# Kernel optimization log

Hardware: AMD Instinct MI355X
Metric: run time of the kernel (lower is better)

Reference implementation:

```python
import jax, jax.numpy as jnp
import numpy as np

NEG_SLOPE = 0.2  # PyG GATConv default negative_slope


def gat_layer(x, edge_index, W, att_src, att_dst, bias):
    """GATConv with self-loops, concat heads. x:[N,F_in], W:[F_in,H*C]."""
    N = x.shape[0]
    H, C = att_src.shape
    loop = jnp.arange(N, dtype=edge_index.dtype)
    src = jnp.concatenate([edge_index[0], loop])  # [E+N]
    dst = jnp.concatenate([edge_index[1], loop])
    h = (x @ W).reshape(N, H, C)                  # [N,H,C]
    a_src = jnp.einsum('nhc,hc->nh', h, att_src)  # [N,H]
    a_dst = jnp.einsum('nhc,hc->nh', h, att_dst)
    e = a_src[src] + a_dst[dst]                   # [E+N,H]
    e = jnp.where(e > 0, e, NEG_SLOPE * e)        # leaky_relu
    # numerically-stable segment softmax over incoming edges of each dst node
    m = jax.ops.segment_max(e, dst, num_segments=N)           # [N,H]
    ex = jnp.exp(e - m[dst])
    denom = jax.ops.segment_sum(ex, dst, num_segments=N)      # [N,H]
    alpha = ex / (denom[dst] + 1e-16)                          # [E+N,H]
    out = jax.ops.segment_sum(h[src] * alpha[:, :, None], dst, num_segments=N)
    return out.reshape(N, H * C) + bias


def setup_inputs() -> dict:
    key = jax.random.key(0)
    ks = jax.random.split(key, 16)
    N, E, F_IN, HID, H, NCLS = 50000, 800000, 128, 64, 4, 40
    HC = H * HID
    s = 0.1
    return {
        'x': jax.random.normal(ks[0], (N, F_IN), jnp.float32),
        'edge_index': jax.random.randint(ks[1], (2, E), 0, N, jnp.int32),
        'W1': jax.random.normal(ks[2], (F_IN, HC), jnp.float32) * s,
        'att_src1': jax.random.normal(ks[3], (H, HID), jnp.float32) * s,
        'att_dst1': jax.random.normal(ks[4], (H, HID), jnp.float32) * s,
        'b1': jnp.zeros((HC,), jnp.float32),
        'W2': jax.random.normal(ks[5], (HC, HC), jnp.float32) * s,
        'att_src2': jax.random.normal(ks[6], (H, HID), jnp.float32) * s,
        'att_dst2': jax.random.normal(ks[7], (H, HID), jnp.float32) * s,
        'b2': jnp.zeros((HC,), jnp.float32),
        'fcW1': jax.random.normal(ks[8], (HC, HID), jnp.float32) * s,
        'fcb1': jnp.zeros((HID,), jnp.float32),
        'fcW2': jax.random.normal(ks[9], (HID, NCLS), jnp.float32) * s,
        'fcb2': jnp.zeros((NCLS,), jnp.float32),
    }


def reference(x, edge_index, W1, att_src1, att_dst1, b1,
              W2, att_src2, att_dst2, b2, fcW1, fcb1, fcW2, fcb2):
    h = gat_layer(x, edge_index, W1, att_src1, att_dst1, b1)
    h = jax.nn.elu(h)
    h = gat_layer(h, edge_index, W2, att_src2, att_dst2, b2)
    h = jax.nn.elu(h)
    h = jnp.maximum(h @ fcW1 + fcb1, 0.0)  # ReLU; dropout is identity in eval
    return h @ fcW2 + fcb2                 # [N, num_classes]
```

## Files before the change

kernel.cpp:

```cpp
#include <hip/hip_runtime.h>

typedef __attribute__((ext_vector_type(8))) _Float16 fp16x8;
typedef __attribute__((ext_vector_type(4))) float f32x4;
typedef unsigned int u32;

__device__ __forceinline__ float lrelu(float x) { return x > 0.f ? x : 0.2f * x; }
__device__ __forceinline__ float elu(float x) { return x > 0.f ? x : __expf(x) - 1.f; }

__device__ __forceinline__ void gl2lds16(const void* g, void* l) {
    __builtin_amdgcn_global_load_lds((const __attribute__((address_space(1))) u32*)g,
                                     (__attribute__((address_space(3))) u32*)l, 16, 0, 0);
}

__device__ __forceinline__ void t16t_body(const float* __restrict__ W, _Float16* __restrict__ T,
                                          int N, int Nreal, int t) {
    int lane = t & 63, rem = t >> 6;
    int kk = rem & 1; rem >>= 1;
    int ncg = N / 16;
    int cg = rem % ncg, kc = rem / ncg;
    int k = kc * 64 + kk * 32 + (lane >> 4) * 8;
    int n = cg * 16 + (lane & 15);
    fp16x8 o;
#pragma unroll
    for (int j = 0; j < 8; ++j)
        o[j] = (n < Nreal) ? (_Float16)W[(size_t)(k + j) * Nreal + n] : (_Float16)0.f;
    *(fp16x8*)(T + (size_t)t * 8) = o;
}

__global__ __launch_bounds__(256) void k_prep(const float* __restrict__ W1, _Float16* __restrict__ W1T,
                                              const float* __restrict__ W2, _Float16* __restrict__ W2T,
                                              const float* __restrict__ fcW1, _Float16* __restrict__ fWT,
                                              const float* __restrict__ fcW2, _Float16* __restrict__ f2T,
                                              const int* __restrict__ dst, int* __restrict__ cnt) {
    int b = blockIdx.x, tid = threadIdx.x;
    if (b < 16)      t16t_body(W1, W1T, 256, 256, b * 256 + tid);
    else if (b < 48) t16t_body(W2, W2T, 256, 256, (b - 16) * 256 + tid);
    else if (b < 56) t16t_body(fcW1, fWT, 64, 64, (b - 48) * 256 + tid);
    else if (b < 58) t16t_body(fcW2, f2T, 64, 40, (b - 56) * 256 + tid);
    else             atomicAdd(&cnt[dst[(b - 58) * 256 + tid]], 1);
}

__global__ __launch_bounds__(256) void k_scan_a(const int* __restrict__ cnt, int* __restrict__ s,
                                                int* __restrict__ partial, int N) {
    __shared__ int sh[256];
    int t = threadIdx.x, gid = blockIdx.x * 256 + t;
    sh[t] = gid < N ? cnt[gid] : 0;
    __syncthreads();
    for (int off = 1; off < 256; off <<= 1) {
        int add = (t >= off) ? sh[t - off] : 0;
        __syncthreads();
        sh[t] += add;
        __syncthreads();
    }
    if (gid < N) s[gid] = sh[t];
    if (t == 255) partial[blockIdx.x] = sh[255];
}
__global__ __launch_bounds__(256) void k_scan_bc(const int* __restrict__ s, const int* __restrict__ partial,
                                                 const int* __restrict__ cnt, int* __restrict__ row_ptr,
                                                 int* __restrict__ cursor, int* __restrict__ bcur, int N) {
    __shared__ int red[256];
    int t = threadIdx.x, bid = blockIdx.x;
    int a = 0;
    for (int i = t; i < bid; i += 256) a += partial[i];
    red[t] = a;
    __syncthreads();
    for (int off = 128; off; off >>= 1) {
        if (t < off) red[t] += red[t + off];
        __syncthreads();
    }
    int base = red[0];
    int gid = bid * 256 + t;
    if (gid >= N) return;
    int val = s[gid] + base;
    row_ptr[gid + 1] = val;
    int excl = val - cnt[gid];
    cursor[gid] = excl;
    if ((gid & 511) == 0) bcur[gid >> 9] = excl;
    if (gid == 0) row_ptr[0] = 0;
}

__global__ __launch_bounds__(256) void k_bin(const int* __restrict__ src, const int* __restrict__ dst,
                                             int* __restrict__ bcur, int2* __restrict__ pairbuf, int E) {
    __shared__ int cnt[128], gbase[128], excl[128], cur2[128], sh[128];
    __shared__ int saddr[1024];
    __shared__ int2 spair[1024];
    const int tid = threadIdx.x;
    const int eb = blockIdx.x * 1024;
    if (tid < 128) { cnt[tid] = 0; cur2[tid] = 0; }
    __syncthreads();
    int s_[4], d_[4];
#pragma unroll
    for (int j = 0; j < 4; ++j) {
        int e = eb + j * 256 + tid;
        if (e < E) {
            s_[j] = src[e]; d_[j] = dst[e];
            atomicAdd(&cnt[d_[j] >> 9], 1);
        } else d_[j] = -1;
    }
    __syncthreads();
    if (tid < 128) sh[tid] = cnt[tid];
    __syncthreads();
    for (int off = 1; off < 128; off <<= 1) {
        int add = 0;
        if (tid < 128 && tid >= off) add = sh[tid - off];
        __syncthreads();
        if (tid < 128) sh[tid] += add;
        __syncthreads();
    }
    if (tid < 128) {
        excl[tid] = sh[tid] - cnt[tid];
        if (cnt[tid] > 0) gbase[tid] = atomicAdd(&bcur[tid], cnt[tid]);
    }
    __syncthreads();
#pragma unroll
    for (int j = 0; j < 4; ++j) {
        if (d_[j] >= 0) {
            int b = d_[j] >> 9;
            int r = atomicAdd(&cur2[b], 1);
            int slot = excl[b] + r;
            spair[slot] = make_int2(s_[j], d_[j]);
            saddr[slot] = gbase[b] + r;
        }
    }
    __syncthreads();
    int tot = min(1024, E - eb);
#pragma unroll
    for (int j = 0; j < 4; ++j) {
        int slot = j * 256 + tid;
        if (slot < tot) pairbuf[saddr[slot]] = spair[slot];
    }
}

template<int KV, int NW, int ATT, int AFP32>
__device__ __forceinline__ void gemm_body(int bid,
              const _Float16* __restrict__ Ah, const float* __restrict__ Af,
              const _Float16* __restrict__ BT, _Float16* __restrict__ Chi,
              const float* __restrict__ att_s, const float* __restrict__ att_d,
              float* __restrict__ a_src, float* __restrict__ a_dst,
              int M, int Nc) {
    constexpr int NCG = NW / 16;
    constexpr int CHUNK = NW * 64;
    constexpr int FPW = (CHUNK / 512) / 8;
    __shared__ _Float16 Bs[CHUNK];
    const int m0 = bid * 128;
    const int tid = threadIdx.x;
    const int lane = tid & 63, wv = tid >> 6;
    const int r16 = lane & 15, quad = lane >> 4;
    const int arow = min(m0 + wv * 16 + r16, M - 1);

    f32x4 acc[NCG];
#pragma unroll
    for (int cg = 0; cg < NCG; ++cg) acc[cg] = (f32x4){0, 0, 0, 0};

    constexpr int NCH = KV / 64;
#pragma unroll
    for (int kc = 0; kc < NCH; ++kc) {
        if (kc) __syncthreads();
#pragma unroll
        for (int f = 0; f < FPW; ++f) {
            int fr = wv * FPW + f;
            gl2lds16(BT + (size_t)kc * CHUNK + fr * 512 + lane * 8, &Bs[fr * 512]);
        }
        fp16x8 ar[2];
        if (AFP32) {
            const float* Ap = Af + (size_t)arow * KV + kc * 64 + quad * 8;
#pragma unroll
            for (int kk = 0; kk < 2; ++kk) {
                float4 u0 = *(const float4*)(Ap + kk * 32);
                float4 u1 = *(const float4*)(Ap + kk * 32 + 4);
                fp16x8 h8;
                h8[0] = (_Float16)u0.x; h8[1] = (_Float16)u0.y;
                h8[2] = (_Float16)u0.z; h8[3] = (_Float16)u0.w;
                h8[4] = (_Float16)u1.x; h8[5] = (_Float16)u1.y;
                h8[6] = (_Float16)u1.z; h8[7] = (_Float16)u1.w;
                ar[kk] = h8;
            }
        } else {
            const _Float16* Ahp = Ah + (size_t)arow * KV + kc * 64 + quad * 8;
#pragma unroll
            for (int kk = 0; kk < 2; ++kk) ar[kk] = *(const fp16x8*)(Ahp + kk * 32);
        }
        __syncthreads();
#pragma unroll
        for (int kk = 0; kk < 2; ++kk) {
#pragma unroll
            for (int cg = 0; cg < NCG; ++cg) {
                fp16x8 bh = *(const fp16x8*)(&Bs[(cg * 2 + kk) * 512 + lane * 8]);
                acc[cg] = __builtin_amdgcn_mfma_f32_16x16x32_f16(ar[kk], bh, acc[cg], 0, 0, 0);
            }
        }
    }

    const int rbase = m0 + wv * 16 + quad * 4;

    if (ATT) {
#pragma unroll
        for (int hq = 0; hq < 4; ++hq) {
            float as[4], ad[4];
#pragma unroll
            for (int cg = 0; cg < 4; ++cg) {
                as[cg] = att_s[hq * 64 + cg * 16 + r16];
                ad[cg] = att_d[hq * 64 + cg * 16 + r16];
            }
#pragma unroll
            for (int i = 0; i < 4; ++i) {
                float ps = acc[hq * 4 + 0][i] * as[0] + acc[hq * 4 + 1][i] * as[1]
                         + acc[hq * 4 + 2][i] * as[2] + acc[hq * 4 + 3][i] * as[3];
                float pd = acc[hq * 4 + 0][i] * ad[0] + acc[hq * 4 + 1][i] * ad[1]
                         + acc[hq * 4 + 2][i] * ad[2] + acc[hq * 4 + 3][i] * ad[3];
#pragma unroll
                for (int d = 1; d < 16; d <<= 1) {
                    ps += __shfl_xor(ps, d);
                    pd += __shfl_xor(pd, d);
                }
                int r = rbase + i;
                if (r16 == 0 && r < M) {
                    a_src[(size_t)r * 4 + hq] = ps;
                    a_dst[(size_t)r * 4 + hq] = pd;
                }
            }
        }
    }

#pragma unroll
    for (int cg = 0; cg < NCG; ++cg) {
        int c = cg * 16 + r16;
        if (c >= Nc) continue;
#pragma unroll
        for (int i = 0; i < 4; ++i) {
            int r = rbase + i;
            if (r < M) Chi[(size_t)r * Nc + c] = (_Float16)acc[cg][i];
        }
    }
}

__global__ __launch_bounds__(512, 4)
void k_work1(const float* __restrict__ x, const _Float16* __restrict__ W1T,
             _Float16* __restrict__ h,
             const float* __restrict__ att_s, const float* __restrict__ att_d,
             float* __restrict__ a_src, float* __restrict__ a_dst,
             const int2* __restrict__ pairbuf,
             int* __restrict__ cursor, int* __restrict__ csr,
             int M, int E, int RB) {
    if ((int)blockIdx.x >= RB) {
        int base = (blockIdx.x - RB) * 2048;
#pragma unroll
        for (int j = 0; j < 4; ++j) {
            int i = base + j * 512 + threadIdx.x;
            if (i < E) {
                int2 p = pairbuf[i];
                int pos = atomicAdd(&cursor[p.y], 1);
                csr[pos] = p.x;
            }
        }
        return;
    }
    gemm_body<128, 256, 1, 1>(blockIdx.x, nullptr, x, W1T, h, att_s, att_d, a_src, a_dst, M, 256);
}

#define AG2_LDA 264
__global__ __launch_bounds__(512, 4) void k_ag2(
        const _Float16* __restrict__ h, const float* __restrict__ a_src,
        const float* __restrict__ a_dst, const int* __restrict__ row_ptr,
        const int* __restrict__ csr, const float* __restrict__ bias,
        const _Float16* __restrict__ BT,
        const float* __restrict__ att_s, const float* __restrict__ att_d,
        float* __restrict__ a_src2, float* __restrict__ a_dst2,
        _Float16* __restrict__ h2, int N) {
    __shared__ _Float16 A[16 * AG2_LDA];
    __shared__ float psp[8][16], pdp[8][16];
    const int tid = threadIdx.x;
    const int n0 = blockIdx.x * 16;

    {
        int r = tid >> 5;
        int n = min(n0 + r, N - 1);
        int cl = tid & 31;
        int hd = cl >> 3;
        int beg = row_ptr[n], end = row_ptr[n + 1];
        float adh = a_dst[(size_t)4 * n + hd];
        const _Float16* hb = h + (size_t)cl * 8;

        float ws = __expf(lrelu(a_src[(size_t)4 * n + hd] + adh));
        fp16x8 sv = *(const fp16x8*)(hb + (size_t)n * 256);
        float acc[8];
#pragma unroll
        for (int j = 0; j < 8; ++j) acc[j] = ws * (float)sv[j];
        float dn = ws;

        int e = beg;
        for (; e + 4 <= end; e += 4) {
            int s0 = csr[e], s1 = csr[e + 1], s2 = csr[e + 2], s3 = csr[e + 3];
            float z0 = a_src[(size_t)4 * s0 + hd], z1 = a_src[(size_t)4 * s1 + hd];
            float z2 = a_src[(size_t)4 * s2 + hd], z3 = a_src[(size_t)4 * s3 + hd];
            fp16x8 v0 = *(const fp16x8*)(hb + (size_t)s0 * 256);
            fp16x8 v1 = *(const fp16x8*)(hb + (size_t)s1 * 256);
            fp16x8 v2 = *(const fp16x8*)(hb + (size_t)s2 * 256);
            fp16x8 v3 = *(const fp16x8*)(hb + (size_t)s3 * 256);
            float w0 = __expf(lrelu(z0 + adh)), w1 = __expf(lrelu(z1 + adh));
            float w2 = __expf(lrelu(z2 + adh)), w3 = __expf(lrelu(z3 + adh));
            dn += (w0 + w1) + (w2 + w3);
#pragma unroll
            for (int j = 0; j < 8; ++j)
                acc[j] += w0 * (float)v0[j] + w1 * (float)v1[j]
                        + w2 * (float)v2[j] + w3 * (float)v3[j];
        }
        for (; e + 2 <= end; e += 2) {
            int s0 = csr[e], s1 = csr[e + 1];
            float z0 = a_src[(size_t)4 * s0 + hd], z1 = a_src[(size_t)4 * s1 + hd];
            fp16x8 v0 = *(const fp16x8*)(hb + (size_t)s0 * 256);
            fp16x8 v1 = *(const fp16x8*)(hb + (size_t)s1 * 256);
            float w0 = __expf(lrelu(z0 + adh)), w1 = __expf(lrelu(z1 + adh));
            dn += w0 + w1;
#pragma unroll
            for (int j = 0; j < 8; ++j)
                acc[j] += w0 * (float)v0[j] + w1 * (float)v1[j];
        }
        if (e < end) {
            int s0 = csr[e];
            float w0 = __expf(lrelu(a_src[(size_t)4 * s0 + hd] + adh));
            fp16x8 v0 = *(const fp16x8*)(hb + (size_t)s0 * 256);
            dn += w0;
#pragma unroll
            for (int j = 0; j < 8; ++j) acc[j] += w0 * (float)v0[j];
        }

        float inv = 1.f / (dn + 1e-16f);
        float4 b0 = *(const float4*)(bias + cl * 8);
        float4 b1v = *(const float4*)(bias + cl * 8 + 4);
        fp16x8 hi;
        hi[0] = (_Float16)elu(acc[0] * inv + b0.x);
        hi[1] = (_Float16)elu(acc[1] * inv + b0.y);
        hi[2] = (_Float16)elu(acc[2] * inv + b0.z);
        hi[3] = (_Float16)elu(acc[3] * inv + b0.w);
        hi[4] = (_Float16)elu(acc[4] * inv + b1v.x);
        hi[5] = (_Float16)elu(acc[5] * inv + b1v.y);
        hi[6] = (_Float16)elu(acc[6] * inv + b1v.z);
        hi[7] = (_Float16)elu(acc[7] * inv + b1v.w);
        *(fp16x8*)(&A[r * AG2_LDA + cl * 8]) = hi;
    }
    __syncthreads();

    const int lane = tid & 63, wv = tid >> 6;
    const int r16 = lane & 15, quad = lane >> 4;
    f32x4 acc2[2];
    acc2[0] = (f32x4){0, 0, 0, 0};
    acc2[1] = (f32x4){0, 0, 0, 0};
#pragma unroll
    for (int kc = 0; kc < 4; ++kc) {
        fp16x8 ar[2];
#pragma unroll
        for (int kk = 0; kk < 2; ++kk)
            ar[kk] = *(const fp16x8*)(&A[r16 * AG2_LDA + kc * 64 + kk * 32 + quad * 8]);
#pragma unroll
        for (int kk = 0; kk < 2; ++kk) {
#pragma unroll
            for (int j = 0; j < 2; ++j) {
                int cg = wv * 2 + j;
                fp16x8 bh = *(const fp16x8*)(BT + ((size_t)(kc * 16 + cg) * 2 + kk) * 512 + lane * 8);
                acc2[j] = __builtin_amdgcn_mfma_f32_16x16x32_f16(ar[kk], bh, acc2[j], 0, 0, 0);
            }
        }
    }
    {
        float as[2], ad[2];
#pragma unroll
        for (int j = 0; j < 2; ++j) {
            int c = (wv * 2 + j) * 16 + r16;
            as[j] = att_s[c];
            ad[j] = att_d[c];
        }
#pragma unroll
        for (int i = 0; i < 4; ++i) {
            float ps = acc2[0][i] * as[0] + acc2[1][i] * as[1];
            float pd = acc2[0][i] * ad[0] + acc2[1][i] * ad[1];
#pragma unroll
            for (int d = 1; d < 16; d <<= 1) {
                ps += __shfl_xor(ps, d);
                pd += __shfl_xor(pd, d);
            }
            if (r16 == 0) {
                psp[wv][quad * 4 + i] = ps;
                pdp[wv][quad * 4 + i] = pd;
            }
        }
    }
#pragma unroll
    for (int j = 0; j < 2; ++j) {
        int c = (wv * 2 + j) * 16 + r16;
#pragma unroll
        for (int i = 0; i < 4; ++i) {
            int rr = n0 + quad * 4 + i;
            if (rr < N) h2[(size_t)rr * 256 + c] = (_Float16)acc2[j][i];
        }
    }
    __syncthreads();
    if (tid < 64) {
        int row = tid >> 2, hq = tid & 3;
        int rr = n0 + row;
        if (rr < N) {
            a_src2[(size_t)rr * 4 + hq] = psp[2 * hq][row] + psp[2 * hq + 1][row];
            a_dst2[(size_t)rr * 4 + hq] = pdp[2 * hq][row] + pdp[2 * hq + 1][row];
        }
    }
}

__global__ __launch_bounds__(256, 4)
void k_fc(const _Float16* __restrict__ Ah, const _Float16* __restrict__ BT1,
          const _Float16* __restrict__ BT2, const float* __restrict__ b1,
          const float* __restrict__ b2, float* __restrict__ out, int M) {
    __shared__ _Float16 S[4096 + 64 * 72];
    const int m0 = blockIdx.x * 64;
    const int tid = threadIdx.x;
    const int lane = tid & 63, wv = tid >> 6;
    const int r16 = lane & 15, quad = lane >> 4;
    const int arow = min(m0 + wv * 16 + r16, M - 1);

    f32x4 acc[4];
#pragma unroll
    for (int cg = 0; cg < 4; ++cg) acc[cg] = (f32x4){0, 0, 0, 0};
#pragma unroll
    for (int kc = 0; kc < 4; ++kc) {
        if (kc) __syncthreads();
#pragma unroll
        for (int f = 0; f < 2; ++f) {
            int fr = wv * 2 + f;
            gl2lds16(BT1 + (size_t)kc * 4096 + fr * 512 + lane * 8, &S[fr * 512]);
        }
        fp16x8 ar[2];
        const _Float16* Ahp = Ah + (size_t)arow * 256 + kc * 64 + quad * 8;
#pragma unroll
        for (int kk = 0; kk < 2; ++kk) ar[kk] = *(const fp16x8*)(Ahp + kk * 32);
        __syncthreads();
#pragma unroll
        for (int kk = 0; kk < 2; ++kk) {
#pragma unroll
            for (int cg = 0; cg < 4; ++cg) {
                fp16x8 bh = *(const fp16x8*)(&S[(cg * 2 + kk) * 512 + lane * 8]);
                acc[cg] = __builtin_amdgcn_mfma_f32_16x16x32_f16(ar[kk], bh, acc[cg], 0, 0, 0);
            }
        }
    }
    __syncthreads();
    const int rloc = wv * 16 + quad * 4;
#pragma unroll
    for (int cg = 0; cg < 4; ++cg) {
        int c = cg * 16 + r16;
        float badd = b1[c];
#pragma unroll
        for (int i = 0; i < 4; ++i)
            S[4096 + (rloc + i) * 72 + c] = (_Float16)fmaxf(acc[cg][i] + badd, 0.f);
    }
    __syncthreads();
    const int arow2 = wv * 16 + r16;
    fp16x8 a2[2];
#pragma unroll
    for (int kk = 0; kk < 2; ++kk)
        a2[kk] = *(const fp16x8*)(&S[4096 + arow2 * 72 + kk * 32 + quad * 8]);
    f32x4 acc2[4];
#pragma unroll
    for (int cg = 0; cg < 4; ++cg) acc2[cg] = (f32x4){0, 0, 0, 0};
#pragma unroll
    for (int kk = 0; kk < 2; ++kk) {
#pragma unroll
        for (int cg = 0; cg < 4; ++cg) {
            fp16x8 bh = *(const fp16x8*)(BT2 + (cg * 2 + kk) * 512 + lane * 8);
            acc2[cg] = __builtin_amdgcn_mfma_f32_16x16x32_f16(a2[kk], bh, acc2[cg], 0, 0, 0);
        }
    }
    const int rbase = m0 + wv * 16 + quad * 4;
#pragma unroll
    for (int cg = 0; cg < 4; ++cg) {
        int c = cg * 16 + r16;
        if (c >= 40) continue;
        float badd = b2[c];
#pragma unroll
        for (int i = 0; i < 4; ++i) {
            int r = rbase + i;
            if (r < M) out[(size_t)r * 40 + c] = acc2[cg][i] + badd;
        }
    }
}

__global__ __launch_bounds__(256) void k_aggr8(const _Float16* __restrict__ h, const float* __restrict__ a_src,
                                               const float* __restrict__ a_dst, const int* __restrict__ row_ptr,
                                               const int* __restrict__ csr, const float* __restrict__ bias,
                                               _Float16* __restrict__ o_hi, int N) {
    int n = blockIdx.x * 8 + (threadIdx.x >> 5);
    if (n >= N) return;
    int cl = threadIdx.x & 31;
    int hd = cl >> 3;
    int beg = row_ptr[n], end = row_ptr[n + 1];
    float adh = a_dst[(size_t)4 * n + hd];
    const _Float16* hb = h + (size_t)cl * 8;

    float ws = __expf(lrelu(a_src[(size_t)4 * n + hd] + adh));
    fp16x8 sv = *(const fp16x8*)(hb + (size_t)n * 256);
    float acc[8];
#pragma unroll
    for (int j = 0; j < 8; ++j) acc[j] = ws * (float)sv[j];
    float dn = ws;

    int e = beg;
    for (; e + 4 <= end; e += 4) {
        int s0 = csr[e], s1 = csr[e + 1], s2 = csr[e + 2], s3 = csr[e + 3];
        float z0 = a_src[(size_t)4 * s0 + hd], z1 = a_src[(size_t)4 * s1 + hd];
        float z2 = a_src[(size_t)4 * s2 + hd], z3 = a_src[(size_t)4 * s3 + hd];
        fp16x8 v0 = *(const fp16x8*)(hb + (size_t)s0 * 256);
        fp16x8 v1 = *(const fp16x8*)(hb + (size_t)s1 * 256);
        fp16x8 v2 = *(const fp16x8*)(hb + (size_t)s2 * 256);
        fp16x8 v3 = *(const fp16x8*)(hb + (size_t)s3 * 256);
        float w0 = __expf(lrelu(z0 + adh)), w1 = __expf(lrelu(z1 + adh));
        float w2 = __expf(lrelu(z2 + adh)), w3 = __expf(lrelu(z3 + adh));
        dn += (w0 + w1) + (w2 + w3);
#pragma unroll
        for (int j = 0; j < 8; ++j)
            acc[j] += w0 * (float)v0[j] + w1 * (float)v1[j]
                    + w2 * (float)v2[j] + w3 * (float)v3[j];
    }
    for (; e + 2 <= end; e += 2) {
        int s0 = csr[e], s1 = csr[e + 1];
        float z0 = a_src[(size_t)4 * s0 + hd], z1 = a_src[(size_t)4 * s1 + hd];
        fp16x8 v0 = *(const fp16x8*)(hb + (size_t)s0 * 256);
        fp16x8 v1 = *(const fp16x8*)(hb + (size_t)s1 * 256);
        float w0 = __expf(lrelu(z0 + adh)), w1 = __expf(lrelu(z1 + adh));
        dn += w0 + w1;
#pragma unroll
        for (int j = 0; j < 8; ++j)
            acc[j] += w0 * (float)v0[j] + w1 * (float)v1[j];
    }
    if (e < end) {
        int s0 = csr[e];
        float w0 = __expf(lrelu(a_src[(size_t)4 * s0 + hd] + adh));
        fp16x8 v0 = *(const fp16x8*)(hb + (size_t)s0 * 256);
        dn += w0;
#pragma unroll
        for (int j = 0; j < 8; ++j) acc[j] += w0 * (float)v0[j];
    }

    float inv = 1.f / (dn + 1e-16f);
    float4 b0 = *(const float4*)(bias + cl * 8);
    float4 b1v = *(const float4*)(bias + cl * 8 + 4);
    fp16x8 hi;
    hi[0] = (_Float16)elu(acc[0] * inv + b0.x);
    hi[1] = (_Float16)elu(acc[1] * inv + b0.y);
    hi[2] = (_Float16)elu(acc[2] * inv + b0.z);
    hi[3] = (_Float16)elu(acc[3] * inv + b0.w);
    hi[4] = (_Float16)elu(acc[4] * inv + b1v.x);
    hi[5] = (_Float16)elu(acc[5] * inv + b1v.y);
    hi[6] = (_Float16)elu(acc[6] * inv + b1v.z);
    hi[7] = (_Float16)elu(acc[7] * inv + b1v.w);
    *(fp16x8*)(o_hi + (size_t)n * 256 + cl * 8) = hi;
}

extern "C" void kernel_launch(void* const* d_in, const int* in_sizes, int n_in,
                              void* d_out, int out_size, void* d_ws, size_t ws_size,
                              hipStream_t stream) {
    const int N = 50000, E = 800000, F_IN = 128, HC = 256, HID = 64, NCLS = 40;
    const float* x    = (const float*)d_in[0];
    const int*   ei   = (const int*)d_in[1];
    const float* W1   = (const float*)d_in[2];
    const float* as1  = (const float*)d_in[3];
    const float* ad1  = (const float*)d_in[4];
    const float* b1   = (const float*)d_in[5];
    const float* W2   = (const float*)d_in[6];
    const float* as2  = (const float*)d_in[7];
    const float* ad2  = (const float*)d_in[8];
    const float* b2   = (const float*)d_in[9];
    const float* fcW1 = (const float*)d_in[10];
    const float* fcb1 = (const float*)d_in[11];
    const float* fcW2 = (const float*)d_in[12];
    const float* fcb2 = (const float*)d_in[13];
    float* out = (float*)d_out;

    char* wp = (char*)d_ws;
    auto alloc = [&](size_t b) { char* p = wp; wp += (b + 255) & ~(size_t)255; return p; };
    _Float16* h     = (_Float16*)alloc((size_t)N * HC * 2);
    _Float16* ohi   = (_Float16*)alloc((size_t)N * HC * 2);
    float*  asrc  = (float*)alloc((size_t)N * 4 * 4);
    float*  adst  = (float*)alloc((size_t)N * 4 * 4);
    float*  asrc2 = (float*)alloc((size_t)N * 4 * 4);
    float*  adst2 = (float*)alloc((size_t)N * 4 * 4);
    _Float16* W1T   = (_Float16*)alloc((size_t)F_IN * HC * 2);
    _Float16* W2T   = (_Float16*)alloc((size_t)HC * HC * 2);
    _Float16* fWT   = (_Float16*)alloc((size_t)HC * HID * 2);
    _Float16* f2T   = (_Float16*)alloc((size_t)HID * HID * 2);
    int* cnt     = (int*)alloc((size_t)N * 4);
    int* sbuf    = (int*)alloc((size_t)N * 4);
    int* part    = (int*)alloc(1024);
    int* row_ptr = (int*)alloc(((size_t)N + 1) * 4);
    int* cursor  = (int*)alloc((size_t)N * 4);
    int* csr     = (int*)alloc((size_t)E * 4);
    int* bcur    = (int*)alloc(128 * 4);
    int2* pairs  = (int2*)alloc((size_t)E * 8);

    const int* src = ei;
    const int* dst = ei + E;

    const int rb = (N + 127) / 128;
    const int node_blocks8 = (N + 7) / 8;
    const int ag2_blocks = (N + 15) / 16;
    const int bin_blocks = (E + 1023) / 1024;
    const int p2_blocks = (E + 2047) / 2048;
    const int fc_blocks = (N + 63) / 64;

    hipMemsetAsync(cnt, 0, (size_t)N * 4, stream);
    k_prep<<<3183, 256, 0, stream>>>(W1, W1T, W2, W2T, fcW1, fWT, fcW2, f2T, dst, cnt);
    int nb = (N + 255) / 256;
    k_scan_a<<<nb, 256, 0, stream>>>(cnt, sbuf, part, N);
    k_scan_bc<<<nb, 256, 0, stream>>>(sbuf, part, cnt, row_ptr, cursor, bcur, N);
    k_bin<<<bin_blocks, 256, 0, stream>>>(src, dst, bcur, pairs, E);
    k_work1<<<rb + p2_blocks, 512, 0, stream>>>(x, W1T, h, as1, ad1, asrc, adst,
                                                pairs, cursor, csr, N, E, rb);
    k_ag2<<<ag2_blocks, 512, 0, stream>>>(h, asrc, adst, row_ptr, csr, b1,
                                          W2T, as2, ad2, asrc2, adst2, ohi, N);
    k_aggr8<<<node_blocks8, 256, 0, stream>>>(ohi, asrc2, adst2, row_ptr, csr, b2, h, N);
    k_fc<<<fc_blocks, 256, 0, stream>>>(h, fWT, f2T, fcb1, fcb2, out, N);
}
```

Baseline: 328.5 us.

## Fuse second GAT aggregation with the two-layer FC head into one kernel

Merges the layer-2 aggregation kernel and the FC MLP kernel into a single kernel. Each block aggregates 16 nodes into LDS, then runs both small MFMA matmuls on that tile and writes the final logits. This removes the global write and re-read of the N×256 fp16 intermediate and one kernel launch. In exchange, the FC stage is split across fewer waves per block (4 then 3 of 8 waves active), and the FC weights are read from global memory per block instead of being staged in LDS.

Measured after the change: 320.3 us. 1.03x faster.

```diff
diff --git a/kernel.cpp b/kernel.cpp
--- a/kernel.cpp
+++ b/kernel.cpp
@@ -405,152 +405,132 @@
     }
 }
 
-__global__ __launch_bounds__(256, 4)
-void k_fc(const _Float16* __restrict__ Ah, const _Float16* __restrict__ BT1,
-          const _Float16* __restrict__ BT2, const float* __restrict__ b1,
-          const float* __restrict__ b2, float* __restrict__ out, int M) {
-    __shared__ _Float16 S[4096 + 64 * 72];
-    const int m0 = blockIdx.x * 64;
+__global__ __launch_bounds__(512, 4) void k_agfc(
+        const _Float16* __restrict__ h, const float* __restrict__ a_src,
+        const float* __restrict__ a_dst, const int* __restrict__ row_ptr,
+        const int* __restrict__ csr, const float* __restrict__ bias,
+        const _Float16* __restrict__ BT1, const _Float16* __restrict__ BT2,
+        const float* __restrict__ fcb1, const float* __restrict__ fcb2,
+        float* __restrict__ out, int N) {
+    __shared__ _Float16 A[16 * AG2_LDA];
+    __shared__ _Float16 T[16 * 72];
     const int tid = threadIdx.x;
+    const int n0 = blockIdx.x * 16;
+
+    {
+        int r = tid >> 5;
+        int n = min(n0 + r, N - 1);
+        int cl = tid & 31;
+        int hd = cl >> 3;
+        int beg = row_ptr[n], end = row_ptr[n + 1];
+        float adh = a_dst[(size_t)4 * n + hd];
+        const _Float16* hb = h + (size_t)cl * 8;
+
+        float ws = __expf(lrelu(a_src[(size_t)4 * n + hd] + adh));
+        fp16x8 sv = *(const fp16x8*)(hb + (size_t)n * 256);
+        float acc[8];
+#pragma unroll
+        for (int j = 0; j < 8; ++j) acc[j] = ws * (float)sv[j];
+        float dn = ws;
+
+        int e = beg;
+        for (; e + 4 <= end; e += 4) {
+            int s0 = csr[e], s1 = csr[e + 1], s2 = csr[e + 2], s3 = csr[e + 3];
+            float z0 = a_src[(size_t)4 * s0 + hd], z1 = a_src[(size_t)4 * s1 + hd];
+            float z2 = a_src[(size_t)4 * s2 + hd], z3 = a_src[(size_t)4 * s3 + hd];
+            fp16x8 v0 = *(const fp16x8*)(hb + (size_t)s0 * 256);
+            fp16x8 v1 = *(const fp16x8*)(hb + (size_t)s1 * 256);
+            fp16x8 v2 = *(const fp16x8*)(hb + (size_t)s2 * 256);
+            fp16x8 v3 = *(const fp16x8*)(hb + (size_t)s3 * 256);
+            float w0 = __expf(lrelu(z0 + adh)), w1 = __expf(lrelu(z1 + adh));
+            float w2 = __expf(lrelu(z2 + adh)), w3 = __expf(lrelu(z3 + adh));
+            dn += (w0 + w1) + (w2 + w3);
+#pragma unroll
+            for (int j = 0; j < 8; ++j)
+                acc[j] += w0 * (float)v0[j] + w1 * (float)v1[j]
+                        + w2 * (float)v2[j] + w3 * (float)v3[j];
+        }
+        for (; e + 2 <= end; e += 2) {
+            int s0 = csr[e], s1 = csr[e + 1];
+            float z0 = a_src[(size_t)4 * s0 + hd], z1 = a_src[(size_t)4 * s1 + hd];
+            fp16x8 v0 = *(const fp16x8*)(hb + (size_t)s0 * 256);
+            fp16x8 v1 = *(const fp16x8*)(hb + (size_t)s1 * 256);
+            float w0 = __expf(lrelu(z0 + adh)), w1 = __expf(lrelu(z1 + adh));
+            dn += w0 + w1;
+#pragma unroll
+            for (int j = 0; j < 8; ++j)
+                acc[j] += w0 * (float)v0[j] + w1 * (float)v1[j];
+        }
+        if (e < end) {
+            int s0 = csr[e];
+            float w0 = __expf(lrelu(a_src[(size_t)4 * s0 + hd] + adh));
+            fp16x8 v0 = *(const fp16x8*)(hb + (size_t)s0 * 256);
+            dn += w0;
+#pragma unroll
+            for (int j = 0; j < 8; ++j) acc[j] += w0 * (float)v0[j];
+        }
+
+        float inv = 1.f / (dn + 1e-16f);
+        float4 b0 = *(const float4*)(bias + cl * 8);
+        float4 b1v = *(const float4*)(bias + cl * 8 + 4);
+        fp16x8 hi;
+        hi[0] = (_Float16)elu(acc[0] * inv + b0.x);
+        hi[1] = (_Float16)elu(acc[1] * inv + b0.y);
+        hi[2] = (_Float16)elu(acc[2] * inv + b0.z);
+        hi[3] = (_Float16)elu(acc[3] * inv + b0.w);
+        hi[4] = (_Float16)elu(acc[4] * inv + b1v.x);
+        hi[5] = (_Float16)elu(acc[5] * inv + b1v.y);
+        hi[6] = (_Float16)elu(acc[6] * inv + b1v.z);
+        hi[7] = (_Float16)elu(acc[7] * inv + b1v.w);
+        *(fp16x8*)(&A[(tid >> 5) * AG2_LDA + cl * 8]) = hi;
+    }
+    __syncthreads();
+
     const int lane = tid & 63, wv = tid >> 6;
     const int r16 = lane & 15, quad = lane >> 4;
-    const int arow = min(m0 + wv * 16 + r16, M - 1);
-
-    f32x4 acc[4];
-#pragma unroll
-    for (int cg = 0; cg < 4; ++cg) acc[cg] = (f32x4){0, 0, 0, 0};
-#pragma unroll
-    for (int kc = 0; kc < 4; ++kc) {
-        if (kc) __syncthreads();
-#pragma unroll
-        for (int f = 0; f < 2; ++f) {
-            int fr = wv * 2 + f;
-            gl2lds16(BT1 + (size_t)kc * 4096 + fr * 512 + lane * 8, &S[fr * 512]);
-        }
-        fp16x8 ar[2];
-        const _Float16* Ahp = Ah + (size_t)arow * 256 + kc * 64 + quad * 8;
-#pragma unroll
-        for (int kk = 0; kk < 2; ++kk) ar[kk] = *(const fp16x8*)(Ahp + kk * 32);
-        __syncthreads();
+    if (wv < 4) {
+        f32x4 acc1 = (f32x4){0, 0, 0, 0};
+#pragma unroll
+        for (int kc = 0; kc < 4; ++kc) {
+            fp16x8 ar[2];
+#pragma unroll
+            for (int kk = 0; kk < 2; ++kk)
+                ar[kk] = *(const fp16x8*)(&A[r16 * AG2_LDA + kc * 64 + kk * 32 + quad * 8]);
+#pragma unroll
+            for (int kk = 0; kk < 2; ++kk) {
+                fp16x8 bh = *(const fp16x8*)(BT1 + ((size_t)(kc * 4 + wv) * 2 + kk) * 512 + lane * 8);
+                acc1 = __builtin_amdgcn_mfma_f32_16x16x32_f16(ar[kk], bh, acc1, 0, 0, 0);
+            }
+        }
+        int c = wv * 16 + r16;
+        float badd = fcb1[c];
+#pragma unroll
+        for (int i = 0; i < 4; ++i)
+            T[(quad * 4 + i) * 72 + c] = (_Float16)fmaxf(acc1[i] + badd, 0.f);
+    }
+    __syncthreads();
+
+    if (wv < 3) {
+        fp16x8 a2[2];
+#pragma unroll
+        for (int kk = 0; kk < 2; ++kk)
+            a2[kk] = *(const fp16x8*)(&T[r16 * 72 + kk * 32 + quad * 8]);
+        f32x4 acc2 = (f32x4){0, 0, 0, 0};
 #pragma unroll
         for (int kk = 0; kk < 2; ++kk) {
-#pragma unroll
-            for (int cg = 0; cg < 4; ++cg) {
-                fp16x8 bh = *(const fp16x8*)(&S[(cg * 2 + kk) * 512 + lane * 8]);
-                acc[cg] = __builtin_amdgcn_mfma_f32_16x16x32_f16(ar[kk], bh, acc[cg], 0, 0, 0);
-            }
-        }
-    }
-    __syncthreads();
-    const int rloc = wv * 16 + quad * 4;
-#pragma unroll
-    for (int cg = 0; cg < 4; ++cg) {
-        int c = cg * 16 + r16;
-        float badd = b1[c];
-#pragma unroll
-        for (int i = 0; i < 4; ++i)
-            S[4096 + (rloc + i) * 72 + c] = (_Float16)fmaxf(acc[cg][i] + badd, 0.f);
-    }
-    __syncthreads();
-    const int arow2 = wv * 16 + r16;
-    fp16x8 a2[2];
-#pragma unroll
-    for (int kk = 0; kk < 2; ++kk)
-        a2[kk] = *(const fp16x8*)(&S[4096 + arow2 * 72 + kk * 32 + quad * 8]);
-    f32x4 acc2[4];
-#pragma unroll
-    for (int cg = 0; cg < 4; ++cg) acc2[cg] = (f32x4){0, 0, 0, 0};
-#pragma unroll
-    for (int kk = 0; kk < 2; ++kk) {
-#pragma unroll
-        for (int cg = 0; cg < 4; ++cg) {
-            fp16x8 bh = *(const fp16x8*)(BT2 + (cg * 2 + kk) * 512 + lane * 8);
-            acc2[cg] = __builtin_amdgcn_mfma_f32_16x16x32_f16(a2[kk], bh, acc2[cg], 0, 0, 0);
-        }
-    }
-    const int rbase = m0 + wv * 16 + quad * 4;
-#pragma unroll
-    for (int cg = 0; cg < 4; ++cg) {
-        int c = cg * 16 + r16;
-        if (c >= 40) continue;
-        float badd = b2[c];
-#pragma unroll
-        for (int i = 0; i < 4; ++i) {
-            int r = rbase + i;
-            if (r < M) out[(size_t)r * 40 + c] = acc2[cg][i] + badd;
-        }
-    }
-}
-
-__global__ __launch_bounds__(256) void k_aggr8(const _Float16* __restrict__ h, const float* __restrict__ a_src,
-                                               const float* __restrict__ a_dst, const int* __restrict__ row_ptr,
-                                               const int* __restrict__ csr, const float* __restrict__ bias,
-                                               _Float16* __restrict__ o_hi, int N) {
-    int n = blockIdx.x * 8 + (threadIdx.x >> 5);
-    if (n >= N) return;
-    int cl = threadIdx.x & 31;
-    int hd = cl >> 3;
-    int beg = row_ptr[n], end = row_ptr[n + 1];
-    float adh = a_dst[(size_t)4 * n + hd];
-    const _Float16* hb = h + (size_t)cl * 8;
-
-    float ws = __expf(lrelu(a_src[(size_t)4 * n + hd] + adh));
-    fp16x8 sv = *(const fp16x8*)(hb + (size_t)n * 256);
-    float acc[8];
-#pragma unroll
-    for (int j = 0; j < 8; ++j) acc[j] = ws * (float)sv[j];
-    float dn = ws;
-
-    int e = beg;
-    for (; e + 4 <= end; e += 4) {
-        int s0 = csr[e], s1 = csr[e + 1], s2 = csr[e + 2], s3 = csr[e + 3];
-        float z0 = a_src[(size_t)4 * s0 + hd], z1 = a_src[(size_t)4 * s1 + hd];
-        float z2 = a_src[(size_t)4 * s2 + hd], z3 = a_src[(size_t)4 * s3 + hd];
-        fp16x8 v0 = *(const fp16x8*)(hb + (size_t)s0 * 256);
-        fp16x8 v1 = *(const fp16x8*)(hb + (size_t)s1 * 256);
-        fp16x8 v2 = *(const fp16x8*)(hb + (size_t)s2 * 256);
-        fp16x8 v3 = *(const fp16x8*)(hb + (size_t)s3 * 256);
-        float w0 = __expf(lrelu(z0 + adh)), w1 = __expf(lrelu(z1 + adh));
-        float w2 = __expf(lrelu(z2 + adh)), w3 = __expf(lrelu(z3 + adh));
-        dn += (w0 + w1) + (w2 + w3);
-#pragma unroll
-        for (int j = 0; j < 8; ++j)
-            acc[j] += w0 * (float)v0[j] + w1 * (float)v1[j]
-                    + w2 * (float)v2[j] + w3 * (float)v3[j];
-    }
-    for (; e + 2 <= end; e += 2) {
-        int s0 = csr[e], s1 = csr[e + 1];
-        float z0 = a_src[(size_t)4 * s0 + hd], z1 = a_src[(size_t)4 * s1 + hd];
-        fp16x8 v0 = *(const fp16x8*)(hb + (size_t)s0 * 256);
-        fp16x8 v1 = *(const fp16x8*)(hb + (size_t)s1 * 256);
-        float w0 = __expf(lrelu(z0 + adh)), w1 = __expf(lrelu(z1 + adh));
-        dn += w0 + w1;
-#pragma unroll
-        for (int j = 0; j < 8; ++j)
-            acc[j] += w0 * (float)v0[j] + w1 * (float)v1[j];
-    }
-    if (e < end) {
-        int s0 = csr[e];
-        float w0 = __expf(lrelu(a_src[(size_t)4 * s0 + hd] + adh));
-        fp16x8 v0 = *(const fp16x8*)(hb + (size_t)s0 * 256);
-        dn += w0;
-#pragma unroll
-        for (int j = 0; j < 8; ++j) acc[j] += w0 * (float)v0[j];
-    }
-
-    float inv = 1.f / (dn + 1e-16f);
-    float4 b0 = *(const float4*)(bias + cl * 8);
-    float4 b1v = *(const float4*)(bias + cl * 8 + 4);
-    fp16x8 hi;
-    hi[0] = (_Float16)elu(acc[0] * inv + b0.x);
-    hi[1] = (_Float16)elu(acc[1] * inv + b0.y);
-    hi[2] = (_Float16)elu(acc[2] * inv + b0.z);
-    hi[3] = (_Float16)elu(acc[3] * inv + b0.w);
-    hi[4] = (_Float16)elu(acc[4] * inv + b1v.x);
-    hi[5] = (_Float16)elu(acc[5] * inv + b1v.y);
-    hi[6] = (_Float16)elu(acc[6] * inv + b1v.z);
-    hi[7] = (_Float16)elu(acc[7] * inv + b1v.w);
-    *(fp16x8*)(o_hi + (size_t)n * 256 + cl * 8) = hi;
+            fp16x8 bh = *(const fp16x8*)(BT2 + ((size_t)wv * 2 + kk) * 512 + lane * 8);
+            acc2 = __builtin_amdgcn_mfma_f32_16x16x32_f16(a2[kk], bh, acc2, 0, 0, 0);
+        }
+        int c = wv * 16 + r16;
+        if (c < 40) {
+            float badd = fcb2[c];
+#pragma unroll
+            for (int i = 0; i < 4; ++i) {
+                int rr = n0 + quad * 4 + i;
+                if (rr < N) out[(size_t)rr * 40 + c] = acc2[i] + badd;
+            }
+        }
+    }
 }
 
 extern "C" void kernel_launch(void* const* d_in, const int* in_sizes, int n_in,
@@ -598,11 +578,9 @@
     const int* dst = ei + E;
 
     const int rb = (N + 127) / 128;
-    const int node_blocks8 = (N + 7) / 8;
-    const int ag2_blocks = (N + 15) / 16;
+    const int ag_blocks = (N + 15) / 16;
     const int bin_blocks = (E + 1023) / 1024;
     const int p2_blocks = (E + 2047) / 2048;
-    const int fc_blocks = (N + 63) / 64;
 
     hipMemsetAsync(cnt, 0, (size_t)N * 4, stream);
     k_prep<<<3183, 256, 0, stream>>>(W1, W1T, W2, W2T, fcW1, fWT, fcW2, f2T, dst, cnt);
@@ -612,8 +590,8 @@
     k_bin<<<bin_blocks, 256, 0, stream>>>(src, dst, bcur, pairs, E);
     k_work1<<<rb + p2_blocks, 512, 0, stream>>>(x, W1T, h, as1, ad1, asrc, adst,
                                                 pairs, cursor, csr, N, E, rb);
-    k_ag2<<<ag2_blocks, 512, 0, stream>>>(h, asrc, adst, row_ptr, csr, b1,
-                                          W2T, as2, ad2, asrc2, adst2, ohi, N);
-    k_aggr8<<<node_blocks8, 256, 0, stream>>>(ohi, asrc2, adst2, row_ptr, csr, b2, h, N);
-    k_fc<<<fc_blocks, 256, 0, stream>>>(h, fWT, f2T, fcb1, fcb2, out, N);
-}
+    k_ag2<<<ag_blocks, 512, 0, stream>>>(h, asrc, adst, row_ptr, csr, b1,
+                                         W2T, as2, ad2, asrc2, adst2, ohi, N);
+    k_agfc<<<ag_blocks, 512, 0, stream>>>(ohi, asrc2, adst2, row_ptr, csr, b2,
+                                          fWT, f2T, fcb1, fcb2, out, N);
+}
```
